# Optimization experiments

Measured on AMD Instinct MI355X. Metric: run time of the kernel, lower is better.

## Reference

```python
import jax, jax.numpy as jnp
import numpy as np
import math

B, H, S, D = 1, 8, 2048, 64
LAMBDA_INIT = 0.8 - 0.6 * math.exp(-0.3)  # depth=1
EPS = 1e-5


def _clin(xr, xi, wr, wi, br, bi):
    # complex linear: (wr + i*wi)(xr + i*xi)
    out_r = xr @ wr.T - xi @ wi.T + br
    out_i = xr @ wi.T + xi @ wr.T + bi
    return out_r, out_i


def setup_inputs() -> dict:
    ks = jax.random.split(jax.random.key(0), 24)
    n = lambda i, shp, s=1.0: jax.random.normal(ks[i], shp, jnp.float32) * s
    inv = 1.0 / math.sqrt(D)
    return {
        'q_r': n(0, (B, H, S, D)), 'q_i': n(1, (B, H, S, D)),
        'k_r': n(2, (B, H, S, D)), 'k_i': n(3, (B, H, S, D)),
        'v_r': n(4, (B, H, S, D)), 'v_i': n(5, (B, H, S, D)),
        'pe_q_r': n(6, (B, H, S, D)), 'pe_q_i': n(7, (B, H, S, D)),
        'pe_k_r': n(8, (B, H, S, D)), 'pe_k_i': n(9, (B, H, S, D)),
        'qwr': n(10, (2 * D, D), inv), 'qwi': n(11, (2 * D, D), inv),
        'qbr': jnp.zeros(2 * D), 'qbi': jnp.zeros(2 * D),
        'kwr': n(12, (D, D), inv), 'kwi': n(13, (D, D), inv),
        'kbr': jnp.zeros(D), 'kbi': jnp.zeros(D),
        'vwr': n(14, (D, D), inv), 'vwi': n(15, (D, D), inv),
        'vbr': jnp.zeros(D), 'vbi': jnp.zeros(D),
        'gwr': n(16, (D, D), inv), 'gwi': n(17, (D, D), inv),
        'gbr': jnp.zeros(D), 'gbi': jnp.zeros(D),
        'owr': n(18, (D, D), inv), 'owi': n(19, (D, D), inv),
        'obr': jnp.zeros(D), 'obi': jnp.zeros(D),
        'lq1': n(20, (H,), 0.1), 'lk1': n(21, (H,), 0.1),
        'lq2': n(22, (H,), 0.1), 'lk2': n(23, (H,), 0.1),
        'subw': jnp.ones(2 * D),
    }


def _forward(q_r, q_i, k_r, k_i, v_r, v_i, pe_q_r, pe_q_i, pe_k_r, pe_k_i,
             qwr, qwi, qbr, qbi, kwr, kwi, kbr, kbi, vwr, vwi, vbr, vbi,
             gwr, gwi, gbr, gbi, owr, owi, obr, obi,
             lq1, lk1, lq2, lk2, subw):
    b, h, s, d = q_r.shape
    scale = d ** (-0.5)
    qpr, qpi = _clin(q_r, q_i, qwr, qwi, qbr, qbi)      # [b,h,s,2d]
    kpr, kpi = _clin(k_r, k_i, kwr, kwi, kbr, kbi)      # [b,h,s,d]
    vpr, vpi = _clin(v_r, v_i, vwr, vwi, vbr, vbi)      # [b,h,s,d]
    qpr = qpr + jnp.concatenate([pe_q_r, pe_q_r], -1)
    qpi = qpi + jnp.concatenate([pe_q_i, pe_q_i], -1)
    kpr = kpr + pe_k_r
    kpi = kpi + pe_k_i
    # split two physical heads: view(..., d, 2) interleaves last dim
    qpr = qpr.reshape(b, h, s, d, 2)
    qpi = qpi.reshape(b, h, s, d, 2)
    q1r, q2r = qpr[..., 0], qpr[..., 1]
    q1i, q2i = qpi[..., 0], qpi[..., 1]

    def attn(qr, qi):
        sr = jnp.einsum('bhqd,bhkd->bhqk', qr, kpr) + jnp.einsum('bhqd,bhkd->bhqk', qi, kpi)
        si = jnp.einsum('bhqd,bhkd->bhqk', qi, kpr) - jnp.einsum('bhqd,bhkd->bhqk', qr, kpi)
        scores = jnp.sqrt(sr * sr + si * si + 1e-8) * scale
        return jax.nn.softmax(scores, axis=-1)

    a1 = attn(q1r, q1i)
    a2 = attn(q2r, q2i)
    o1r = a1 @ vpr; o1i = a1 @ vpi
    o2r = a2 @ vpr; o2i = a2 @ vpi
    # NOTE: torch computes a lambda-weighted difference here but immediately
    # overwrites it with the normed slice below, so it never reaches the output.
    cr = jnp.stack([o1r, o2r], -1).reshape(b, h, s, 2 * d)
    ci = jnp.stack([o1i, o2i], -1).reshape(b, h, s, 2 * d)
    rms = jnp.sqrt(jnp.mean(cr * cr + ci * ci, axis=-1, keepdims=True) + EPS)
    nr = cr / rms * subw
    ni = ci / rms * subw
    ar = nr[..., :d]
    ai = ni[..., :d]
    gr, gi = _clin(q_r, q_i, gwr, gwi, gbr, gbi)
    xr = gr * ar - gi * ai
    xi = gr * ai + gi * ar
    out_r, out_i = _clin(xr, xi, owr, owi, obr, obi)
    return out_r, out_i, gr, gi


def reference(q_r, q_i, k_r, k_i, v_r, v_i, pe_q_r, pe_q_i, pe_k_r, pe_k_i,
              qwr, qwi, qbr, qbi, kwr, kwi, kbr, kbi, vwr, vwi, vbr, vbi,
              gwr, gwi, gbr, gbi, owr, owi, obr, obi,
              lq1, lk1, lq2, lk2, subw):
    return _forward(q_r, q_i, k_r, k_i, v_r, v_i, pe_q_r, pe_q_i, pe_k_r, pe_k_i,
                    qwr, qwi, qbr, qbi, kwr, kwi, kbr, kbi, vwr, vwi, vbr, vbi,
                    gwr, gwi, gbr, gbi, owr, owi, obr, obi,
                    lq1, lk1, lq2, lk2, subw)
```

## Files before the change

kernel.cpp:

```cpp
#include <hip/hip_runtime.h>
#include <hip/hip_bf16.h>

#define NH 8
#define SQ 2048
#define HD 64
#define NTOT (NH * SQ * HD)
#define PIT 72

typedef unsigned short u16;
typedef unsigned int u32;
typedef __attribute__((ext_vector_type(8))) unsigned short us8;
typedef __attribute__((ext_vector_type(4))) unsigned short us4v;
typedef __attribute__((ext_vector_type(8))) _Float16 h8;
typedef __attribute__((ext_vector_type(4))) float f4;
typedef __attribute__((ext_vector_type(4))) u32 u4;

#define MFMA_F16 __builtin_amdgcn_mfma_f32_16x16x32_f16

__device__ __forceinline__ u16 f2h(float f) {
    union { _Float16 h; u16 u; } c; c.h = (_Float16)f; return c.u;
}
__device__ __forceinline__ float h2f(u16 u) {
    union { _Float16 h; u16 u; } c; c.u = u; return (float)c.h;
}
__device__ __forceinline__ h8 neg_h8(h8 a) {
    union { h8 h; u4 u; } c; c.h = a;
    c.u ^= 0x80008000u;
    return c.h;
}
__device__ __forceinline__ h8 pack8h(const float* p) {
    float4 a = ((const float4*)p)[0];
    float4 b = ((const float4*)p)[1];
    h8 r;
    r[0] = (_Float16)a.x; r[1] = (_Float16)a.y; r[2] = (_Float16)a.z; r[3] = (_Float16)a.w;
    r[4] = (_Float16)b.x; r[5] = (_Float16)b.y; r[6] = (_Float16)b.z; r[7] = (_Float16)b.w;
    return r;
}

__device__ __forceinline__ int swz8(int row, int chunk) {
    return row * 64 + ((chunk ^ (row & 7)) << 3);
}

struct Afrag { h8 r0, r1, i0, i1, ni0, ni1; };

__global__ __launch_bounds__(256) void proj_kernel(
    const float* __restrict__ q_r, const float* __restrict__ q_i,
    const float* __restrict__ k_r, const float* __restrict__ k_i,
    const float* __restrict__ v_r, const float* __restrict__ v_i,
    const float* __restrict__ pe_q_r, const float* __restrict__ pe_q_i,
    const float* __restrict__ pe_k_r, const float* __restrict__ pe_k_i,
    const float* __restrict__ qwr, const float* __restrict__ qwi,
    const float* __restrict__ qbr, const float* __restrict__ qbi,
    const float* __restrict__ kwr, const float* __restrict__ kwi,
    const float* __restrict__ kbr, const float* __restrict__ kbi,
    const float* __restrict__ vwr, const float* __restrict__ vwi,
    const float* __restrict__ vbr, const float* __restrict__ vbi,
    const float* __restrict__ gwr, const float* __restrict__ gwi,
    const float* __restrict__ gbr, const float* __restrict__ gbi,
    u16* __restrict__ q1r, u16* __restrict__ q1i,
    u16* __restrict__ q2r, u16* __restrict__ q2i,
    u16* __restrict__ kpr, u16* __restrict__ kpi,
    u16* __restrict__ vtr, u16* __restrict__ vti,
    float* __restrict__ out_gr, float* __restrict__ out_gi)
{
    const int t = threadIdx.x;
    const int wv = t >> 6, l = t & 63;
    const int quad = l >> 4, m16 = l & 15;
    const int rowbase = blockIdx.x * 16;
    const int arow = rowbase + m16;
    const int h = rowbase >> 11;
    const int c0 = quad * 8;

    auto loadA = [&](const float* pr, const float* pi) {
        Afrag a;
        const float* rp = pr + arow * 64;
        const float* ip = pi + arow * 64;
        a.r0 = pack8h(rp + c0);      a.r1 = pack8h(rp + 32 + c0);
        a.i0 = pack8h(ip + c0);      a.i1 = pack8h(ip + 32 + c0);
        a.ni0 = neg_h8(a.i0);        a.ni1 = neg_h8(a.i1);
        return a;
    };

    auto ctile = [&](const Afrag& A, const float* wr, const float* wi, int cb,
                     f4& Cr, f4& Ci) {
        const float* wrp = wr + (cb + m16) * 64;
        const float* wip = wi + (cb + m16) * 64;
        h8 Br0 = pack8h(wrp + c0), Br1 = pack8h(wrp + 32 + c0);
        h8 Bi0 = pack8h(wip + c0), Bi1 = pack8h(wip + 32 + c0);
        Cr = (f4)0.f; Ci = (f4)0.f;
        Cr = MFMA_F16(A.r0,  Br0, Cr, 0, 0, 0);
        Cr = MFMA_F16(A.r1,  Br1, Cr, 0, 0, 0);
        Cr = MFMA_F16(A.ni0, Bi0, Cr, 0, 0, 0);
        Cr = MFMA_F16(A.ni1, Bi1, Cr, 0, 0, 0);
        Ci = MFMA_F16(A.r0,  Bi0, Ci, 0, 0, 0);
        Ci = MFMA_F16(A.r1,  Bi1, Ci, 0, 0, 0);
        Ci = MFMA_F16(A.i0,  Br0, Ci, 0, 0, 0);
        Ci = MFMA_F16(A.i1,  Br1, Ci, 0, 0, 0);
    };

    auto qtile = [&](const Afrag& A, int nt) {
        f4 Cr, Ci;
        ctile(A, qwr, qwi, nt * 16, Cr, Ci);
        int c = nt * 16 + m16;
        float br = qbr[c], bi = qbi[c];
        int dd = c >> 1, pc = c & 63;
        u16* dR = (c & 1) ? q2r : q1r;
        u16* dI = (c & 1) ? q2i : q1i;
        #pragma unroll
        for (int r = 0; r < 4; ++r) {
            int g = rowbase + quad * 4 + r;
            dR[g * 64 + dd] = f2h(Cr[r] + br + pe_q_r[g * 64 + pc]);
            dI[g * 64 + dd] = f2h(Ci[r] + bi + pe_q_i[g * 64 + pc]);
        }
    };
    auto ktile = [&](const Afrag& A, int nt) {
        f4 Cr, Ci;
        ctile(A, kwr, kwi, nt * 16, Cr, Ci);
        int c = nt * 16 + m16;
        float br = kbr[c], bi = kbi[c];
        #pragma unroll
        for (int r = 0; r < 4; ++r) {
            int g = rowbase + quad * 4 + r;
            kpr[g * 64 + c] = f2h(Cr[r] + br + pe_k_r[g * 64 + c]);
            kpi[g * 64 + c] = f2h(Ci[r] + bi + pe_k_i[g * 64 + c]);
        }
    };
    auto vtile = [&](const Afrag& A, int nt) {
        f4 Cr, Ci;
        ctile(A, vwr, vwi, nt * 16, Cr, Ci);
        int c = nt * 16 + m16;
        float br = vbr[c], bi = vbi[c];
        int s0 = (rowbase & 2047) + quad * 4;
        size_t tix = (size_t)(h * 64 + c) * 2048 + s0;
        us4v pr, pi;
        #pragma unroll
        for (int r = 0; r < 4; ++r) {
            pr[r] = f2h(Cr[r] + br);
            pi[r] = f2h(Ci[r] + bi);
        }
        *(us4v*)&vtr[tix] = pr;
        *(us4v*)&vti[tix] = pi;
    };
    auto gtile = [&](const Afrag& A, int nt) {
        f4 Cr, Ci;
        ctile(A, gwr, gwi, nt * 16, Cr, Ci);
        int c = nt * 16 + m16;
        float br = gbr[c], bi = gbi[c];
        #pragma unroll
        for (int r = 0; r < 4; ++r) {
            int g = rowbase + quad * 4 + r;
            out_gr[g * 64 + c] = Cr[r] + br;
            out_gi[g * 64 + c] = Ci[r] + bi;
        }
    };

    if (wv == 0) {
        Afrag Aq = loadA(q_r, q_i);
        qtile(Aq, 0); qtile(Aq, 1); qtile(Aq, 2); qtile(Aq, 3); qtile(Aq, 4);
    } else if (wv == 1) {
        Afrag Aq = loadA(q_r, q_i);
        qtile(Aq, 5); qtile(Aq, 6); qtile(Aq, 7);
        gtile(Aq, 0); gtile(Aq, 1);
    } else if (wv == 2) {
        Afrag Ak = loadA(k_r, k_i);
        ktile(Ak, 0); ktile(Ak, 1); ktile(Ak, 2); ktile(Ak, 3);
        Afrag Aq = loadA(q_r, q_i);
        gtile(Aq, 2);
    } else {
        Afrag Av = loadA(v_r, v_i);
        vtile(Av, 0); vtile(Av, 1); vtile(Av, 2); vtile(Av, 3);
        Afrag Aq = loadA(q_r, q_i);
        gtile(Aq, 3);
    }
}

__global__ __launch_bounds__(512, 2) void attn_kernel(
    const u16* __restrict__ q1r, const u16* __restrict__ q1i,
    const u16* __restrict__ q2r, const u16* __restrict__ q2i,
    const u16* __restrict__ kpr, const u16* __restrict__ kpi,
    const u16* __restrict__ vtr, const u16* __restrict__ vti,
    u16* __restrict__ o1r, u16* __restrict__ o1i,
    u16* __restrict__ o2r, u16* __restrict__ o2i)
{
    __shared__ __align__(16) u16 Kr[2][64 * 64], Ki[2][64 * 64];
    __shared__ __align__(16) u16 Vr[2][64 * 64], Vi[2][64 * 64];
    __shared__ __align__(16) u16 Pb[128 * 64];

    const int t  = threadIdx.x;
    const int qt = blockIdx.x;
    const int h  = blockIdx.z;

    const int wq   = t >> 6;
    const int br   = wq >> 2;
    const int wr   = wq & 3;
    const int l    = t & 63;
    const int quad = l >> 4;
    const int m    = l & 15;

    const u16* Qsr = br ? q2r : q1r;
    const u16* Qsi = br ? q2i : q1i;
    const int hbase = h * SQ * 64;
    const int qbase = hbase + qt * 64 * 64;
    const int vbase = h * 64 * SQ;

    const u16* qrr = Qsr + qbase + (wr * 16 + m) * 64;
    const u16* qri = Qsi + qbase + (wr * 16 + m) * 64;
    h8 Qr0 = *(const h8*)(qrr + quad * 8);
    h8 Qr1 = *(const h8*)(qrr + 32 + quad * 8);
    h8 Qi0 = *(const h8*)(qri + quad * 8);
    h8 Qi1 = *(const h8*)(qri + 32 + quad * 8);
    h8 nQr0 = neg_h8(Qr0);
    h8 nQr1 = neg_h8(Qr1);

    const int sr0 = t >> 3;
    const int sc  = t & 7;
    us8 rK, rC, rV, rW;

    auto issue = [&](int kt) {
        const int kb = hbase + kt * 4096;
        const int vb = vbase + kt * 64;
        const int sc8 = sc * 8;
        rK = *(const us8*)(kpr + kb + sr0 * 64 + sc8);
        rC = *(const us8*)(kpi + kb + sr0 * 64 + sc8);
        rV = *(const us8*)(vtr + vb + sr0 * SQ + sc8);
        rW = *(const us8*)(vti + vb + sr0 * SQ + sc8);
    };
    auto commit = [&](int b) {
        const int o = swz8(sr0, sc);
        *(us8*)&Kr[b][o] = rK;
        *(us8*)&Ki[b][o] = rC;
        *(us8*)&Vr[b][o] = rV;
        *(us8*)&Vi[b][o] = rW;
    };

    float mreg[4], Lp[4];
    #pragma unroll
    for (int r = 0; r < 4; ++r) { mreg[r] = -1e30f; Lp[r] = 0.f; }
    f4 Ovr[4], Ovi[4];
    #pragma unroll
    for (int d = 0; d < 4; ++d) { Ovr[d] = (f4)0.f; Ovi[d] = (f4)0.f; }

    issue(0);
    commit(0);
    issue(1);
    __syncthreads();

    for (int kt = 0; kt < 32; ++kt) {
        const int cur = kt & 1;
        if (kt < 31) commit(cur ^ 1);
        if (kt < 30) issue(kt + 2);

        float sv[4][4];
        #pragma unroll
        for (int nt = 0; nt < 4; ++nt) {
            const int kr = nt * 16 + m;
            h8 k0 = *(const h8*)&Kr[cur][swz8(kr, quad)];
            h8 k1 = *(const h8*)&Kr[cur][swz8(kr, quad + 4)];
            h8 c0 = *(const h8*)&Ki[cur][swz8(kr, quad)];
            h8 c1 = *(const h8*)&Ki[cur][swz8(kr, quad + 4)];
            f4 ar = (f4)0.f, ai = (f4)0.f;
            __builtin_amdgcn_s_setprio(1);
            ar = MFMA_F16(Qr0, k0, ar, 0, 0, 0);
            ar = MFMA_F16(Qr1, k1, ar, 0, 0, 0);
            ar = MFMA_F16(Qi0, c0, ar, 0, 0, 0);
            ar = MFMA_F16(Qi1, c1, ar, 0, 0, 0);
            ai = MFMA_F16(Qi0, k0, ai, 0, 0, 0);
            ai = MFMA_F16(Qi1, k1, ai, 0, 0, 0);
            ai = MFMA_F16(nQr0, c0, ai, 0, 0, 0);
            ai = MFMA_F16(nQr1, c1, ai, 0, 0, 0);
            __builtin_amdgcn_s_setprio(0);
            #pragma unroll
            for (int r = 0; r < 4; ++r)
                sv[nt][r] = __builtin_amdgcn_sqrtf(ar[r] * ar[r] + ai[r] * ai[r] + 1e-8f) * 0.125f;
        }

        float rv[4];
        #pragma unroll
        for (int r = 0; r < 4; ++r) {
            float x = fmaxf(fmaxf(sv[0][r], sv[1][r]), fmaxf(sv[2][r], sv[3][r]));
            x = fmaxf(x, __shfl_xor(x, 1));
            x = fmaxf(x, __shfl_xor(x, 2));
            x = fmaxf(x, __shfl_xor(x, 4));
            x = fmaxf(x, __shfl_xor(x, 8));
            rv[r] = x;
        }

        bool need = (rv[0] > mreg[0] + 8.f) | (rv[1] > mreg[1] + 8.f) |
                    (rv[2] > mreg[2] + 8.f) | (rv[3] > mreg[3] + 8.f);
        if (__any(need)) {
            #pragma unroll
            for (int r = 0; r < 4; ++r) {
                float mn = fmaxf(mreg[r], rv[r]);
                float al = __expf(mreg[r] - mn);
                mreg[r] = mn;
                Lp[r] *= al;
                #pragma unroll
                for (int dtr = 0; dtr < 4; ++dtr) { Ovr[dtr][r] *= al; Ovi[dtr][r] *= al; }
            }
        }

        #pragma unroll
        for (int r = 0; r < 4; ++r) {
            const int prow = wq * 16 + quad * 4 + r;
            #pragma unroll
            for (int nt = 0; nt < 4; ++nt) {
                float p = __expf(sv[nt][r] - mreg[r]);
                Lp[r] += p;
                const int col = nt * 16 + m;
                Pb[swz8(prow, col >> 3) + (col & 7)] = f2h(p);
            }
        }

        const int qrow = wq * 16 + m;
        h8 pa0 = *(const h8*)&Pb[swz8(qrow, quad)];
        h8 pa1 = *(const h8*)&Pb[swz8(qrow, quad + 4)];

        #pragma unroll
        for (int dt = 0; dt < 4; ++dt) {
            const int vr_ = dt * 16 + m;
            h8 b0 = *(const h8*)&Vr[cur][swz8(vr_, quad)];
            h8 b1 = *(const h8*)&Vr[cur][swz8(vr_, quad + 4)];
            h8 d0 = *(const h8*)&Vi[cur][swz8(vr_, quad)];
            h8 d1 = *(const h8*)&Vi[cur][swz8(vr_, quad + 4)];
            __builtin_amdgcn_s_setprio(1);
            Ovr[dt] = MFMA_F16(pa0, b0, Ovr[dt], 0, 0, 0);
            Ovr[dt] = MFMA_F16(pa1, b1, Ovr[dt], 0, 0, 0);
            Ovi[dt] = MFMA_F16(pa0, d0, Ovi[dt], 0, 0, 0);
            Ovi[dt] = MFMA_F16(pa1, d1, Ovi[dt], 0, 0, 0);
            __builtin_amdgcn_s_setprio(0);
        }

        __syncthreads();
    }

    {
        #pragma unroll
        for (int r = 0; r < 4; ++r) {
            float x = Lp[r];
            x += __shfl_xor(x, 1);
            x += __shfl_xor(x, 2);
            x += __shfl_xor(x, 4);
            x += __shfl_xor(x, 8);
            Lp[r] = x;
        }
        u16* Dr = br ? o2r : o1r;
        u16* Di = br ? o2i : o1i;
        float inv[4];
        #pragma unroll
        for (int r = 0; r < 4; ++r) inv[r] = 1.f / Lp[r];
        #pragma unroll
        for (int dt = 0; dt < 4; ++dt) {
            #pragma unroll
            for (int r = 0; r < 4; ++r) {
                int q = wr * 16 + quad * 4 + r;
                Dr[qbase + q * 64 + dt * 16 + m] = f2h(Ovr[dt][r] * inv[r]);
                Di[qbase + q * 64 + dt * 16 + m] = f2h(Ovi[dt][r] * inv[r]);
            }
        }
    }
}

__global__ __launch_bounds__(256) void epi_kernel(
    const u16* __restrict__ o1r, const u16* __restrict__ o1i,
    const u16* __restrict__ o2r, const u16* __restrict__ o2i,
    const float* __restrict__ out_gr, const float* __restrict__ out_gi,
    const float* __restrict__ subw,
    const float* __restrict__ owr, const float* __restrict__ owi,
    const float* __restrict__ obr, const float* __restrict__ obi,
    float* __restrict__ out_r, float* __restrict__ out_i)
{
    __shared__ __align__(16) u16 L1r[16][64], L1i[16][64];
    __shared__ __align__(16) u16 L2r[16][64], L2i[16][64];
    __shared__ __align__(16) u16 Xr[16][PIT], Xi[16][PIT];

    const int t = threadIdx.x;
    const int rowbase = blockIdx.x * 16;

    {
        int r = t >> 4, c4 = (t & 15) * 4;
        size_t gi = (size_t)(rowbase + r) * 64 + c4;
        *(us4v*)&L1r[r][c4] = *(const us4v*)(o1r + gi);
        *(us4v*)&L1i[r][c4] = *(const us4v*)(o1i + gi);
        *(us4v*)&L2r[r][c4] = *(const us4v*)(o2r + gi);
        *(us4v*)&L2i[r][c4] = *(const us4v*)(o2i + gi);
    }
    __syncthreads();

    {
        int r = t >> 4, c4 = (t & 15) * 4;
        float ss = 0.f;
        #pragma unroll
        for (int j = 0; j < 4; ++j) {
            float a = h2f(L1r[r][c4 + j]), b = h2f(L1i[r][c4 + j]);
            float c = h2f(L2r[r][c4 + j]), d = h2f(L2i[r][c4 + j]);
            ss += a * a + b * b + c * c + d * d;
        }
        ss += __shfl_xor(ss, 1);
        ss += __shfl_xor(ss, 2);
        ss += __shfl_xor(ss, 4);
        ss += __shfl_xor(ss, 8);
        float inv = 1.f / sqrtf(ss * (1.f / 128.f) + 1e-5f);

        float4 g_r = *(const float4*)(out_gr + (size_t)(rowbase + r) * 64 + c4);
        float4 g_i = *(const float4*)(out_gi + (size_t)(rowbase + r) * 64 + c4);
        const float* grv = (const float*)&g_r;
        const float* giv = (const float*)&g_i;

        us4v xrp, xip;
        #pragma unroll
        for (int j = 0; j < 4; ++j) {
            int c = c4 + j;
            int s = c >> 1;
            float cr_ = (c & 1) ? h2f(L2r[r][s]) : h2f(L1r[r][s]);
            float ci_ = (c & 1) ? h2f(L2i[r][s]) : h2f(L1i[r][s]);
            float sw = subw[c];
            float ar_ = cr_ * inv * sw;
            float ai_ = ci_ * inv * sw;
            xrp[j] = f2h(grv[j] * ar_ - giv[j] * ai_);
            xip[j] = f2h(grv[j] * ai_ + giv[j] * ar_);
        }
        *(us4v*)&Xr[r][c4] = xrp;
        *(us4v*)&Xi[r][c4] = xip;
    }
    __syncthreads();

    const int wv = t >> 6, l = t & 63;
    const int quad = l >> 4, m16 = l & 15;
    const int c0 = quad * 8;

    h8 Ar0 = *(const h8*)&Xr[m16][c0];
    h8 Ar1 = *(const h8*)&Xr[m16][32 + c0];
    h8 Ai0 = *(const h8*)&Xi[m16][c0];
    h8 Ai1 = *(const h8*)&Xi[m16][32 + c0];
    h8 nAi0 = neg_h8(Ai0), nAi1 = neg_h8(Ai1);

    const int c = wv * 16 + m16;
    const float* wrp = owr + c * 64;
    const float* wip = owi + c * 64;
    h8 Br0 = pack8h(wrp + c0), Br1 = pack8h(wrp + 32 + c0);
    h8 Bi0 = pack8h(wip + c0), Bi1 = pack8h(wip + 32 + c0);

    f4 Cr = (f4)0.f, Ci = (f4)0.f;
    Cr = MFMA_F16(Ar0,  Br0, Cr, 0, 0, 0);
    Cr = MFMA_F16(Ar1,  Br1, Cr, 0, 0, 0);
    Cr = MFMA_F16(nAi0, Bi0, Cr, 0, 0, 0);
    Cr = MFMA_F16(nAi1, Bi1, Cr, 0, 0, 0);
    Ci = MFMA_F16(Ar0,  Bi0, Ci, 0, 0, 0);
    Ci = MFMA_F16(Ar1,  Bi1, Ci, 0, 0, 0);
    Ci = MFMA_F16(Ai0,  Br0, Ci, 0, 0, 0);
    Ci = MFMA_F16(Ai1,  Br1, Ci, 0, 0, 0);

    float br_ = obr[c], bi_ = obi[c];
    #pragma unroll
    for (int r = 0; r < 4; ++r) {
        size_t g = (size_t)(rowbase + quad * 4 + r) * 64 + c;
        out_r[g] = Cr[r] + br_;
        out_i[g] = Ci[r] + bi_;
    }
}

extern "C" void kernel_launch(void* const* d_in, const int* in_sizes, int n_in,
                              void* d_out, int out_size, void* d_ws, size_t ws_size,
                              hipStream_t stream)
{
    (void)in_sizes; (void)n_in; (void)out_size; (void)ws_size;

    float* out    = (float*)d_out;
    float* out_r  = out;
    float* out_i  = out + (size_t)NTOT;
    float* out_gr = out + 2 * (size_t)NTOT;
    float* out_gi = out + 3 * (size_t)NTOT;

    char* w = (char*)d_ws;
    const size_t N = (size_t)NTOT;
    u16* q1r = (u16*)w; w += N * 2;
    u16* q1i = (u16*)w; w += N * 2;
    u16* q2r = (u16*)w; w += N * 2;
    u16* q2i = (u16*)w; w += N * 2;
    u16* kpr = (u16*)w; w += N * 2;
    u16* kpi = (u16*)w; w += N * 2;
    u16* vtr = (u16*)w; w += N * 2;
    u16* vti = (u16*)w; w += N * 2;
    u16* o1r = (u16*)w; w += N * 2;
    u16* o1i = (u16*)w; w += N * 2;
    u16* o2r = (u16*)w; w += N * 2;
    u16* o2i = (u16*)w; w += N * 2;

    proj_kernel<<<dim3(1024), dim3(256), 0, stream>>>(
        (const float*)d_in[0], (const float*)d_in[1],
        (const float*)d_in[2], (const float*)d_in[3],
        (const float*)d_in[4], (const float*)d_in[5],
        (const float*)d_in[6], (const float*)d_in[7],
        (const float*)d_in[8], (const float*)d_in[9],
        (const float*)d_in[10], (const float*)d_in[11],
        (const float*)d_in[12], (const float*)d_in[13],
        (const float*)d_in[14], (const float*)d_in[15],
        (const float*)d_in[16], (const float*)d_in[17],
        (const float*)d_in[18], (const float*)d_in[19],
        (const float*)d_in[20], (const float*)d_in[21],
        (const float*)d_in[22], (const float*)d_in[23],
        (const float*)d_in[24], (const float*)d_in[25],
        q1r, q1i, q2r, q2i, kpr, kpi, vtr, vti, out_gr, out_gi);

    attn_kernel<<<dim3(SQ / 64, 1, NH), dim3(512), 0, stream>>>(
        q1r, q1i, q2r, q2i, kpr, kpi, vtr, vti, o1r, o1i, o2r, o2i);

    epi_kernel<<<dim3(1024), dim3(256), 0, stream>>>(
        o1r, o1i, o2r, o2i, out_gr, out_gi,
        (const float*)d_in[34], (const float*)d_in[26], (const float*)d_in[27],
        (const float*)d_in[28], (const float*)d_in[29],
        out_r, out_i);
}
```

Before: 247.8 us.

## Pre-pack projection weights to fp16 MFMA fragments and stage inputs in LDS

Adds small prep kernels that convert every weight matrix once into fp16, laid out in MFMA B-fragment order, inside workspace scratch. The proj and epilogue kernels then load these packed fragments with single vector loads instead of re-reading and converting fp32 weights in every block. The proj kernel also stages the q/k/v input tiles through swizzled LDS so the q tile, which several waves reuse, is read from global memory once per block. The cost is two extra kernel launches and reuse of the o1r/q1r scratch buffers, which is safe only because of the ordering of the kernels on the stream.

```diff
diff --git a/kernel.cpp b/kernel.cpp
--- a/kernel.cpp
+++ b/kernel.cpp
@@ -5,7 +5,6 @@
 #define SQ 2048
 #define HD 64
 #define NTOT (NH * SQ * HD)
-#define PIT 72
 
 typedef unsigned short u16;
 typedef unsigned int u32;
@@ -43,19 +42,52 @@
 
 struct Afrag { h8 r0, r1, i0, i1, ni0, ni1; };
 
+__global__ __launch_bounds__(128) void prep1_kernel(
+    const float* __restrict__ qwr, const float* __restrict__ qwi,
+    const float* __restrict__ kwr, const float* __restrict__ kwi,
+    const float* __restrict__ vwr, const float* __restrict__ vwi,
+    const float* __restrict__ gwr, const float* __restrict__ gwi,
+    u16* __restrict__ pk)
+{
+    const int b = blockIdx.x;
+    const float* W; int nt;
+    if (b < 8)       { W = qwr; nt = b; }
+    else if (b < 16) { W = qwi; nt = b - 8; }
+    else if (b < 20) { W = kwr; nt = b - 16; }
+    else if (b < 24) { W = kwi; nt = b - 20; }
+    else if (b < 28) { W = vwr; nt = b - 24; }
+    else if (b < 32) { W = vwi; nt = b - 28; }
+    else if (b < 36) { W = gwr; nt = b - 32; }
+    else             { W = gwi; nt = b - 36; }
+    const int t = threadIdx.x, hf = t >> 6, l = t & 63;
+    const int quad = l >> 4, m16 = l & 15;
+    h8 v = pack8h(W + (nt * 16 + m16) * 64 + hf * 32 + quad * 8);
+    *(h8*)(pk + b * 1024 + hf * 512 + l * 8) = v;
+}
+
+__global__ __launch_bounds__(128) void prep2_kernel(
+    const float* __restrict__ owr, const float* __restrict__ owi,
+    u16* __restrict__ pk)
+{
+    const int b = blockIdx.x;
+    const float* W = (b < 4) ? owr : owi;
+    const int nt = b & 3;
+    const int t = threadIdx.x, hf = t >> 6, l = t & 63;
+    const int quad = l >> 4, m16 = l & 15;
+    h8 v = pack8h(W + (nt * 16 + m16) * 64 + hf * 32 + quad * 8);
+    *(h8*)(pk + b * 1024 + hf * 512 + l * 8) = v;
+}
+
 __global__ __launch_bounds__(256) void proj_kernel(
     const float* __restrict__ q_r, const float* __restrict__ q_i,
     const float* __restrict__ k_r, const float* __restrict__ k_i,
     const float* __restrict__ v_r, const float* __restrict__ v_i,
     const float* __restrict__ pe_q_r, const float* __restrict__ pe_q_i,
     const float* __restrict__ pe_k_r, const float* __restrict__ pe_k_i,
-    const float* __restrict__ qwr, const float* __restrict__ qwi,
+    const u16* __restrict__ pk,
     const float* __restrict__ qbr, const float* __restrict__ qbi,
-    const float* __restrict__ kwr, const float* __restrict__ kwi,
     const float* __restrict__ kbr, const float* __restrict__ kbi,
-    const float* __restrict__ vwr, const float* __restrict__ vwi,
     const float* __restrict__ vbr, const float* __restrict__ vbi,
-    const float* __restrict__ gwr, const float* __restrict__ gwi,
     const float* __restrict__ gbr, const float* __restrict__ gbi,
     u16* __restrict__ q1r, u16* __restrict__ q1i,
     u16* __restrict__ q2r, u16* __restrict__ q2i,
@@ -63,30 +95,51 @@
     u16* __restrict__ vtr, u16* __restrict__ vti,
     float* __restrict__ out_gr, float* __restrict__ out_gi)
 {
+    __shared__ __align__(16) u16 Sqr[16 * 64], Sqi[16 * 64];
+    __shared__ __align__(16) u16 Skr[16 * 64], Ski[16 * 64];
+    __shared__ __align__(16) u16 Svr[16 * 64], Svi[16 * 64];
+
     const int t = threadIdx.x;
     const int wv = t >> 6, l = t & 63;
     const int quad = l >> 4, m16 = l & 15;
     const int rowbase = blockIdx.x * 16;
-    const int arow = rowbase + m16;
     const int h = rowbase >> 11;
-    const int c0 = quad * 8;
-
-    auto loadA = [&](const float* pr, const float* pi) {
+    const int l8 = l * 8;
+
+    {
+        const int r = t >> 4, c4 = (t & 15) * 4;
+        const int off = swz8(r, c4 >> 3) + (c4 & 7);
+        const size_t gi = (size_t)(rowbase + r) * 64 + c4;
+        auto stage = [&](const float* src, u16* dst) {
+            float4 v = *(const float4*)(src + gi);
+            us4v p;
+            p[0] = f2h(v.x); p[1] = f2h(v.y); p[2] = f2h(v.z); p[3] = f2h(v.w);
+            *(us4v*)&dst[off] = p;
+        };
+        stage(q_r, Sqr); stage(q_i, Sqi);
+        stage(k_r, Skr); stage(k_i, Ski);
+        stage(v_r, Svr); stage(v_i, Svi);
+    }
+    __syncthreads();
+
+    auto loadA = [&](const u16* Sr, const u16* Si) {
         Afrag a;
-        const float* rp = pr + arow * 64;
-        const float* ip = pi + arow * 64;
-        a.r0 = pack8h(rp + c0);      a.r1 = pack8h(rp + 32 + c0);
-        a.i0 = pack8h(ip + c0);      a.i1 = pack8h(ip + 32 + c0);
-        a.ni0 = neg_h8(a.i0);        a.ni1 = neg_h8(a.i1);
+        a.r0 = *(const h8*)&Sr[swz8(m16, quad)];
+        a.r1 = *(const h8*)&Sr[swz8(m16, quad + 4)];
+        a.i0 = *(const h8*)&Si[swz8(m16, quad)];
+        a.i1 = *(const h8*)&Si[swz8(m16, quad + 4)];
+        a.ni0 = neg_h8(a.i0);
+        a.ni1 = neg_h8(a.i1);
         return a;
     };
 
-    auto ctile = [&](const Afrag& A, const float* wr, const float* wi, int cb,
-                     f4& Cr, f4& Ci) {
-        const float* wrp = wr + (cb + m16) * 64;
-        const float* wip = wi + (cb + m16) * 64;
-        h8 Br0 = pack8h(wrp + c0), Br1 = pack8h(wrp + 32 + c0);
-        h8 Bi0 = pack8h(wip + c0), Bi1 = pack8h(wip + 32 + c0);
+    auto ctile = [&](const Afrag& A, int planeR, int planeI, f4& Cr, f4& Ci) {
+        const u16* pR = pk + planeR * 1024;
+        const u16* pI = pk + planeI * 1024;
+        h8 Br0 = *(const h8*)(pR + l8);
+        h8 Br1 = *(const h8*)(pR + 512 + l8);
+        h8 Bi0 = *(const h8*)(pI + l8);
+        h8 Bi1 = *(const h8*)(pI + 512 + l8);
         Cr = (f4)0.f; Ci = (f4)0.f;
         Cr = MFMA_F16(A.r0,  Br0, Cr, 0, 0, 0);
         Cr = MFMA_F16(A.r1,  Br1, Cr, 0, 0, 0);
@@ -100,7 +153,7 @@
 
     auto qtile = [&](const Afrag& A, int nt) {
         f4 Cr, Ci;
-        ctile(A, qwr, qwi, nt * 16, Cr, Ci);
+        ctile(A, nt, 8 + nt, Cr, Ci);
         int c = nt * 16 + m16;
         float br = qbr[c], bi = qbi[c];
         int dd = c >> 1, pc = c & 63;
@@ -115,7 +168,7 @@
     };
     auto ktile = [&](const Afrag& A, int nt) {
         f4 Cr, Ci;
-        ctile(A, kwr, kwi, nt * 16, Cr, Ci);
+        ctile(A, 16 + nt, 20 + nt, Cr, Ci);
         int c = nt * 16 + m16;
         float br = kbr[c], bi = kbi[c];
         #pragma unroll
@@ -127,7 +180,7 @@
     };
     auto vtile = [&](const Afrag& A, int nt) {
         f4 Cr, Ci;
-        ctile(A, vwr, vwi, nt * 16, Cr, Ci);
+        ctile(A, 24 + nt, 28 + nt, Cr, Ci);
         int c = nt * 16 + m16;
         float br = vbr[c], bi = vbi[c];
         int s0 = (rowbase & 2047) + quad * 4;
@@ -143,7 +196,7 @@
     };
     auto gtile = [&](const Afrag& A, int nt) {
         f4 Cr, Ci;
-        ctile(A, gwr, gwi, nt * 16, Cr, Ci);
+        ctile(A, 32 + nt, 36 + nt, Cr, Ci);
         int c = nt * 16 + m16;
         float br = gbr[c], bi = gbi[c];
         #pragma unroll
@@ -155,21 +208,21 @@
     };
 
     if (wv == 0) {
-        Afrag Aq = loadA(q_r, q_i);
+        Afrag Aq = loadA(Sqr, Sqi);
         qtile(Aq, 0); qtile(Aq, 1); qtile(Aq, 2); qtile(Aq, 3); qtile(Aq, 4);
     } else if (wv == 1) {
-        Afrag Aq = loadA(q_r, q_i);
+        Afrag Aq = loadA(Sqr, Sqi);
         qtile(Aq, 5); qtile(Aq, 6); qtile(Aq, 7);
         gtile(Aq, 0); gtile(Aq, 1);
     } else if (wv == 2) {
-        Afrag Ak = loadA(k_r, k_i);
+        Afrag Ak = loadA(Skr, Ski);
         ktile(Ak, 0); ktile(Ak, 1); ktile(Ak, 2); ktile(Ak, 3);
-        Afrag Aq = loadA(q_r, q_i);
+        Afrag Aq = loadA(Sqr, Sqi);
         gtile(Aq, 2);
     } else {
-        Afrag Av = loadA(v_r, v_i);
+        Afrag Av = loadA(Svr, Svi);
         vtile(Av, 0); vtile(Av, 1); vtile(Av, 2); vtile(Av, 3);
-        Afrag Aq = loadA(q_r, q_i);
+        Afrag Aq = loadA(Sqr, Sqi);
         gtile(Aq, 3);
     }
 }
@@ -365,13 +418,13 @@
     const u16* __restrict__ o2r, const u16* __restrict__ o2i,
     const float* __restrict__ out_gr, const float* __restrict__ out_gi,
     const float* __restrict__ subw,
-    const float* __restrict__ owr, const float* __restrict__ owi,
+    const u16* __restrict__ pko,
     const float* __restrict__ obr, const float* __restrict__ obi,
     float* __restrict__ out_r, float* __restrict__ out_i)
 {
     __shared__ __align__(16) u16 L1r[16][64], L1i[16][64];
     __shared__ __align__(16) u16 L2r[16][64], L2i[16][64];
-    __shared__ __align__(16) u16 Xr[16][PIT], Xi[16][PIT];
+    __shared__ __align__(16) u16 Xr[16 * 64], Xi[16 * 64];
 
     const int t = threadIdx.x;
     const int rowbase = blockIdx.x * 16;
@@ -419,26 +472,27 @@
             xrp[j] = f2h(grv[j] * ar_ - giv[j] * ai_);
             xip[j] = f2h(grv[j] * ai_ + giv[j] * ar_);
         }
-        *(us4v*)&Xr[r][c4] = xrp;
-        *(us4v*)&Xi[r][c4] = xip;
+        const int off = swz8(r, c4 >> 3) + (c4 & 7);
+        *(us4v*)&Xr[off] = xrp;
+        *(us4v*)&Xi[off] = xip;
     }
     __syncthreads();
 
     const int wv = t >> 6, l = t & 63;
     const int quad = l >> 4, m16 = l & 15;
-    const int c0 = quad * 8;
-
-    h8 Ar0 = *(const h8*)&Xr[m16][c0];
-    h8 Ar1 = *(const h8*)&Xr[m16][32 + c0];
-    h8 Ai0 = *(const h8*)&Xi[m16][c0];
-    h8 Ai1 = *(const h8*)&Xi[m16][32 + c0];
+    const int l8 = l * 8;
+
+    h8 Ar0 = *(const h8*)&Xr[swz8(m16, quad)];
+    h8 Ar1 = *(const h8*)&Xr[swz8(m16, quad + 4)];
+    h8 Ai0 = *(const h8*)&Xi[swz8(m16, quad)];
+    h8 Ai1 = *(const h8*)&Xi[swz8(m16, quad + 4)];
     h8 nAi0 = neg_h8(Ai0), nAi1 = neg_h8(Ai1);
 
     const int c = wv * 16 + m16;
-    const float* wrp = owr + c * 64;
-    const float* wip = owi + c * 64;
-    h8 Br0 = pack8h(wrp + c0), Br1 = pack8h(wrp + 32 + c0);
-    h8 Bi0 = pack8h(wip + c0), Bi1 = pack8h(wip + 32 + c0);
+    h8 Br0 = *(const h8*)(pko + wv * 1024 + l8);
+    h8 Br1 = *(const h8*)(pko + wv * 1024 + 512 + l8);
+    h8 Bi0 = *(const h8*)(pko + 4096 + wv * 1024 + l8);
+    h8 Bi1 = *(const h8*)(pko + 4096 + wv * 1024 + 512 + l8);
 
     f4 Cr = (f4)0.f, Ci = (f4)0.f;
     Cr = MFMA_F16(Ar0,  Br0, Cr, 0, 0, 0);
@@ -486,28 +540,38 @@
     u16* o2r = (u16*)w; w += N * 2;
     u16* o2i = (u16*)w; w += N * 2;
 
+    u16* pk1 = o1r;
+    u16* pk2 = q1r;
+
+    prep1_kernel<<<dim3(40), dim3(128), 0, stream>>>(
+        (const float*)d_in[10], (const float*)d_in[11],
+        (const float*)d_in[14], (const float*)d_in[15],
+        (const float*)d_in[18], (const float*)d_in[19],
+        (const float*)d_in[22], (const float*)d_in[23],
+        pk1);
+
     proj_kernel<<<dim3(1024), dim3(256), 0, stream>>>(
         (const float*)d_in[0], (const float*)d_in[1],
         (const float*)d_in[2], (const float*)d_in[3],
         (const float*)d_in[4], (const float*)d_in[5],
         (const float*)d_in[6], (const float*)d_in[7],
         (const float*)d_in[8], (const float*)d_in[9],
-        (const float*)d_in[10], (const float*)d_in[11],
+        pk1,
         (const float*)d_in[12], (const float*)d_in[13],
-        (const float*)d_in[14], (const float*)d_in[15],
         (const float*)d_in[16], (const float*)d_in[17],
-        (const float*)d_in[18], (const float*)d_in[19],
         (const float*)d_in[20], (const float*)d_in[21],
-        (const float*)d_in[22], (const float*)d_in[23],
         (const float*)d_in[24], (const float*)d_in[25],
         q1r, q1i, q2r, q2i, kpr, kpi, vtr, vti, out_gr, out_gi);
 
     attn_kernel<<<dim3(SQ / 64, 1, NH), dim3(512), 0, stream>>>(
         q1r, q1i, q2r, q2i, kpr, kpi, vtr, vti, o1r, o1i, o2r, o2i);
 
+    prep2_kernel<<<dim3(8), dim3(128), 0, stream>>>(
+        (const float*)d_in[26], (const float*)d_in[27], pk2);
+
     epi_kernel<<<dim3(1024), dim3(256), 0, stream>>>(
         o1r, o1i, o2r, o2i, out_gr, out_gi,
-        (const float*)d_in[34], (const float*)d_in[26], (const float*)d_in[27],
+        (const float*)d_in[34], pk2,
         (const float*)d_in[28], (const float*)d_in[29],
         out_r, out_i);
 }
```

Result: faster. 236.1 us (-4.7%).
